# Optimization experiments

Measured on AMD Instinct MI355X. Metric: run time of the kernel, lower is better.

## Reference

```python
import jax, jax.numpy as jnp
import numpy as np

N = 4096        # nodes (cells)
E = 131072      # edges (avg degree 32)
IN = 3000       # input features (genes)
HID = 128       # hidden dim per head
H = 4           # attention heads
LAT = 16        # latent dim
NEG_SLOPE = 0.2 # PyG GATConv leaky_relu slope


def _gat_sparse(x, src, dst, W, a_src, a_dst, b, concat):
    """PyG GATConv on an edge list (src -> dst, softmax grouped by dst)."""
    n = x.shape[0]
    h_, c = a_src.shape
    h = (x @ W).reshape(n, h_, c)                      # [N,H,C]
    e_src = (h * a_src[None]).sum(-1)                  # [N,H]
    e_dst = (h * a_dst[None]).sum(-1)                  # [N,H]
    e = jax.nn.leaky_relu(e_src[src] + e_dst[dst], NEG_SLOPE)  # [E,H]
    m = jax.ops.segment_max(e, dst, num_segments=n)
    ex = jnp.exp(e - m[dst])
    denom = jax.ops.segment_sum(ex, dst, num_segments=n)
    alpha = ex / (denom[dst] + 1e-16)                  # PyG softmax eps
    out = jax.ops.segment_sum(alpha[:, :, None] * h[src], dst, num_segments=n)
    out = out.reshape(n, h_ * c) if concat else out.mean(1)
    return out + b


def _gat_dense(x, W, a_src, a_dst, b, concat):
    """GATConv over the complete graph (the SVD low-rank reconstruction is
    generically fully dense, so to_sparse() keeps all N^2 entries; with
    used_edge_weight=False only the structure matters)."""
    n = x.shape[0]
    h_, c = a_src.shape
    h = (x @ W).reshape(n, h_, c)
    e_src = (h * a_src[None]).sum(-1)                  # [N,H]
    e_dst = (h * a_dst[None]).sum(-1)                  # [N,H]
    # scores[i (target), j (source), head]
    scores = jax.nn.leaky_relu(e_dst[:, None, :] + e_src[None, :, :], NEG_SLOPE)
    alpha = jax.nn.softmax(scores, axis=1)             # softmax over sources
    out = jnp.einsum('ijh,jhc->ihc', alpha, h)
    out = out.reshape(n, h_ * c) if concat else out.mean(1)
    return out + b


def setup_inputs() -> dict:
    key = jax.random.key(0)
    ks = jax.random.split(key, 16)
    s = 0.05
    x = jax.random.normal(ks[0], (N, IN), jnp.float32)
    src = jax.random.randint(ks[1], (E,), 0, N, jnp.int32)
    off = jax.random.randint(ks[2], (E,), 1, N, jnp.int32)
    dst = (src + off) % N                              # no self loops (PyG re-adds them)
    edge_index = jnp.stack([src, dst], axis=0)
    edge_attr = jax.random.uniform(ks[3], (E,), jnp.float32)
    D1 = H * HID
    return {
        'x': x, 'edge_index': edge_index, 'edge_attr': edge_attr,
        'W1': jax.random.normal(ks[4], (IN, D1), jnp.float32) * s,
        'a1_src': jax.random.normal(ks[5], (H, HID), jnp.float32) * s,
        'a1_dst': jax.random.normal(ks[6], (H, HID), jnp.float32) * s,
        'b1': jnp.zeros((D1,), jnp.float32),
        'Wm': jax.random.normal(ks[7], (D1, H * LAT), jnp.float32) * s,
        'am_src': jax.random.normal(ks[8], (H, LAT), jnp.float32) * s,
        'am_dst': jax.random.normal(ks[9], (H, LAT), jnp.float32) * s,
        'bm': jnp.zeros((LAT,), jnp.float32),
        'Ws': jax.random.normal(ks[10], (D1, H * LAT), jnp.float32) * s,
        'as_src': jax.random.normal(ks[11], (H, LAT), jnp.float32) * s,
        'as_dst': jax.random.normal(ks[12], (H, LAT), jnp.float32) * s,
        'bs': jnp.zeros((LAT,), jnp.float32),
    }


def reference(x, edge_index, edge_attr, W1, a1_src, a1_dst, b1,
              Wm, am_src, am_dst, bm, Ws, as_src, as_dst, bs):
    loops = jnp.arange(N, dtype=edge_index.dtype)
    src = jnp.concatenate([edge_index[0], loops])      # GATConv add_self_loops=True
    dst = jnp.concatenate([edge_index[1], loops])
    # branch 1: original sparse graph
    x1 = _gat_sparse(x, src, dst, W1, a1_src, a1_dst, b1, True)
    z_mean1 = _gat_sparse(x1, src, dst, Wm, am_src, am_dst, bm, False)
    z_log_std1 = _gat_sparse(x1, src, dst, Ws, as_src, as_dst, bs, False)
    # branch 2: SVD low-rank reconstructed adjacency => complete graph
    x2 = _gat_dense(x, W1, a1_src, a1_dst, b1, True)
    z_mean2 = _gat_dense(x2, Wm, am_src, am_dst, bm, False)
    z_log_std2 = _gat_dense(x2, Ws, as_src, as_dst, bs, False)
    return (z_mean1, z_log_std1, z_mean2, z_log_std2)
```

## Files before the change

kernel.cpp:

```cpp
#include <hip/hip_runtime.h>

typedef unsigned short u16;
typedef unsigned long long u64;
typedef __attribute__((ext_vector_type(8))) short short8;
typedef __attribute__((ext_vector_type(4))) float f32x4;

#define NN   4096
#define EE   131072
#define ETOT (EE + NN)
#define HH   4
#define IND  3000
#define KP   3008
#define D1   512
#define C1   128
#define C2   16

__device__ __forceinline__ float b2f(u16 u){
  union { unsigned int i; float f; } v; v.i = ((unsigned int)u) << 16; return v.f;
}
__device__ __forceinline__ u16 f2b(float f){
  unsigned int x = __float_as_uint(f);
  unsigned int r = (x + 0x7fffu + ((x >> 16) & 1u)) >> 16;
  return (u16)r;
}
__device__ __forceinline__ float lrelu(float x){ return x > 0.f ? x : 0.2f * x; }

__device__ __forceinline__ void glds16(const void* g, void* l){
  __builtin_amdgcn_global_load_lds(
      (const __attribute__((address_space(1))) unsigned int*)g,
      (__attribute__((address_space(3))) unsigned int*)l, 16, 0, 0);
}

__global__ void zero_out_kernel(float* p, int n){
  int i = blockIdx.x * blockDim.x + threadIdx.x;
  if (i < n) p[i] = 0.f;
}

__global__ __launch_bounds__(256) void cvtXW_kernel(const float* __restrict__ X,
    const float* __restrict__ W, u16* __restrict__ Xhi, u16* __restrict__ Xlo,
    u16* __restrict__ Whi, u16* __restrict__ Wlo){
  __shared__ float T[64][65];
  int b = blockIdx.x;
  if (b < 6016){
    int id = b * 256 + threadIdx.x;
    int m = id / 376, ch = id - m * 376;
    int k = ch * 8;
    float v[8];
    if (k + 8 <= IND){
      float4 a = *(const float4*)(X + (size_t)m * IND + k);
      float4 bb = *(const float4*)(X + (size_t)m * IND + k + 4);
      v[0]=a.x; v[1]=a.y; v[2]=a.z; v[3]=a.w; v[4]=bb.x; v[5]=bb.y; v[6]=bb.z; v[7]=bb.w;
    } else {
      #pragma unroll
      for (int j = 0; j < 8; ++j){ int kk = k + j; v[j] = (kk < IND) ? X[(size_t)m*IND + kk] : 0.f; }
    }
    u16 h8[8], l8[8];
    #pragma unroll
    for (int j = 0; j < 8; ++j){ h8[j] = f2b(v[j]); l8[j] = f2b(v[j] - b2f(h8[j])); }
    *(uint4*)(Xhi + (size_t)m * KP + k) = *(uint4*)h8;
    *(uint4*)(Xlo + (size_t)m * KP + k) = *(uint4*)l8;
  } else {
    int wb = b - 6016;
    int kb = wb % 47, nb = wb / 47;
    int k0 = kb * 64, n0 = nb * 64;
    int t = threadIdx.x;
    #pragma unroll
    for (int rr = 0; rr < 4; ++rr){
      int kl = (t >> 4) + rr * 16;
      int nn = (t & 15) * 4;
      int k = k0 + kl;
      float4 v = make_float4(0.f, 0.f, 0.f, 0.f);
      if (k < IND) v = *(const float4*)(W + (size_t)k * D1 + n0 + nn);
      T[kl][nn] = v.x; T[kl][nn+1] = v.y; T[kl][nn+2] = v.z; T[kl][nn+3] = v.w;
    }
    __syncthreads();
    int nloc = t >> 2, kseg = (t & 3) * 16;
    int n = n0 + nloc;
    #pragma unroll
    for (int c2 = 0; c2 < 2; ++c2){
      int kloc = kseg + c2 * 8;
      u16 h8[8], l8[8];
      #pragma unroll
      for (int j = 0; j < 8; ++j){
        float f = T[kloc + j][nloc];
        h8[j] = f2b(f); l8[j] = f2b(f - b2f(h8[j]));
      }
      *(uint4*)(Whi + (size_t)n * KP + k0 + kloc) = *(uint4*)h8;
      *(uint4*)(Wlo + (size_t)n * KP + k0 + kloc) = *(uint4*)l8;
    }
  }
}

__global__ __launch_bounds__(256) void cvtW2_kernel(const float* __restrict__ WM,
    const float* __restrict__ WS, u16* __restrict__ Wh, u16* __restrict__ Wl){
  __shared__ float T[64][65];
  int half = blockIdx.y;
  int k0 = blockIdx.x * 64;
  const float* W = half ? WS : WM;
  int t = threadIdx.x;
  #pragma unroll
  for (int p = 0; p < 4; ++p){
    int r = p * 16 + (t >> 4), c4 = (t & 15) * 4;
    float4 v = *(const float4*)(W + (size_t)(k0 + r) * 64 + c4);
    T[r][c4] = v.x; T[r][c4+1] = v.y; T[r][c4+2] = v.z; T[r][c4+3] = v.w;
  }
  __syncthreads();
  #pragma unroll
  for (int p = 0; p < 4; ++p){
    int n = p * 16 + (t >> 4), k4 = (t & 15) * 4;
    u16 h4[4], l4[4];
    #pragma unroll
    for (int j = 0; j < 4; ++j){
      float f = T[k4 + j][n];
      h4[j] = f2b(f); l4[j] = f2b(f - b2f(h4[j]));
    }
    size_t o = (size_t)(half * 64 + n) * 512 + k0 + k4;
    *(ushort4*)(Wh + o) = *(ushort4*)h4;
    *(ushort4*)(Wl + o) = *(ushort4*)l4;
  }
}

__global__ __launch_bounds__(512) void gemm_mfma(const u16* __restrict__ Xhi,
    const u16* __restrict__ Xlo, const u16* __restrict__ Whi, const u16* __restrict__ Wlo,
    float* __restrict__ Hh){
  __shared__ u16 sbuf[2][4][4096];
  int t = threadIdx.x, lane = t & 63;
  int wv = __builtin_amdgcn_readfirstlane(t >> 6);
  int ksw = wv >> 2;
  int wr = (wv >> 1) & 1, wc = wv & 1;
  int bm = blockIdx.x * 64, bn = blockIdx.y * 64;
  f32x4 acc[2][2] = {};
  int srow = t >> 3;
  int sc = (t & 7) ^ (srow & 7);
  const char* gAh = (const char*)(Xhi + (size_t)(bm + srow) * KP) + sc * 16;
  const char* gAl = (const char*)(Xlo + (size_t)(bm + srow) * KP) + sc * 16;
  const char* gBh = (const char*)(Whi + (size_t)(bn + srow) * KP) + sc * 16;
  const char* gBl = (const char*)(Wlo + (size_t)(bn + srow) * KP) + sc * 16;
  int r16 = lane & 15, kq = lane >> 4;
  int cc = ksw * 4 + kq;
  int aoff[2], boff[2];
  #pragma unroll
  for (int m = 0; m < 2; ++m){
    int arow = wr * 32 + m * 16 + r16;
    aoff[m] = arow * 128 + ((cc ^ (arow & 7)) * 16);
  }
  #pragma unroll
  for (int n = 0; n < 2; ++n){
    int brow = wc * 32 + n * 16 + r16;
    boff[n] = brow * 128 + ((cc ^ (brow & 7)) * 16);
  }

  #define STAGE(step, b) do { int ko = (step) * 128;            \
      glds16(gAh + ko, (char*)sbuf[b][0] + t * 16);             \
      glds16(gAl + ko, (char*)sbuf[b][1] + t * 16);             \
      glds16(gBh + ko, (char*)sbuf[b][2] + t * 16);             \
      glds16(gBl + ko, (char*)sbuf[b][3] + t * 16);             \
    } while (0)
  #define BARRIER()  asm volatile("s_barrier" ::: "memory")
  #define WAIT_V4()  asm volatile("s_waitcnt vmcnt(4)" ::: "memory")
  #define WAIT_V0()  asm volatile("s_waitcnt vmcnt(0)" ::: "memory")

  STAGE(0, 0);
  STAGE(1, 1);
  WAIT_V4();
  BARRIER();
  for (int i = 0; i < 47; ++i){
    int cur = i & 1;
    const char* pAh = (const char*)sbuf[cur][0];
    const char* pAl = (const char*)sbuf[cur][1];
    const char* pBh = (const char*)sbuf[cur][2];
    const char* pBl = (const char*)sbuf[cur][3];
    short8 ah[2], al[2], bh[2], bl[2];
    #pragma unroll
    for (int m = 0; m < 2; ++m){
      ah[m] = *(const short8*)(pAh + aoff[m]);
      al[m] = *(const short8*)(pAl + aoff[m]);
    }
    #pragma unroll
    for (int n = 0; n < 2; ++n){
      bh[n] = *(const short8*)(pBh + boff[n]);
      bl[n] = *(const short8*)(pBl + boff[n]);
    }
    #pragma unroll
    for (int m = 0; m < 2; ++m)
      #pragma unroll
      for (int n = 0; n < 2; ++n){
        acc[m][n] = __builtin_amdgcn_mfma_f32_16x16x32_bf16(ah[m], bh[n], acc[m][n], 0, 0, 0);
        acc[m][n] = __builtin_amdgcn_mfma_f32_16x16x32_bf16(ah[m], bl[n], acc[m][n], 0, 0, 0);
        acc[m][n] = __builtin_amdgcn_mfma_f32_16x16x32_bf16(al[m], bh[n], acc[m][n], 0, 0, 0);
      }
    BARRIER();
    if (i + 2 < 47){
      STAGE(i + 2, cur);
      WAIT_V4();
    } else {
      WAIT_V0();
    }
    BARRIER();
  }
  #undef STAGE
  #undef BARRIER
  #undef WAIT_V4
  #undef WAIT_V0
  float* red = (float*)sbuf;
  int pp = wr * 2 + wc;
  if (ksw){
    #pragma unroll
    for (int m = 0; m < 2; ++m)
      #pragma unroll
      for (int n = 0; n < 2; ++n)
        #pragma unroll
        for (int r = 0; r < 4; ++r)
          red[((((m*2+n)*4 + r) << 8) + (pp << 6)) + lane] = acc[m][n][r];
  }
  __syncthreads();
  if (!ksw){
    #pragma unroll
    for (int m = 0; m < 2; ++m)
      #pragma unroll
      for (int n = 0; n < 2; ++n){
        #pragma unroll
        for (int r = 0; r < 4; ++r)
          acc[m][n][r] += red[((((m*2+n)*4 + r) << 8) + (pp << 6)) + lane];
        int row = bm + wr * 32 + m * 16 + kq * 4;
        int col = bn + wc * 32 + n * 16 + r16;
        float* o = Hh + (size_t)row * D1 + col;
        #pragma unroll
        for (int r = 0; r < 4; ++r) o[(size_t)r * D1] = acc[m][n][r];
      }
  }
}

__global__ __launch_bounds__(256) void gemm_h_split(const float* __restrict__ X,
    const float* __restrict__ Wc, float* __restrict__ Hh){
  __shared__ u16 Ahs[64][40], Als[64][40], Bhs[64][40], Bls[64][40];
  int t = threadIdx.x, lane = t & 63, wave = t >> 6;
  int wr = wave >> 1, wcc = wave & 1;
  int bm = blockIdx.x * 64, bn = blockIdx.y * 64;
  f32x4 acc[2][2] = {};
  int arow = t >> 2, akc = (t & 3) << 3;
  int brow = t >> 3, bnc = (t & 7) << 3;
  for (int k0 = 0; k0 < IND; k0 += 32){
    float va[8];
    size_t abase = (size_t)(bm + arow) * IND + k0 + akc;
    if (k0 + akc + 8 <= IND){
      float4 r0 = *(const float4*)(X + abase);
      float4 r1 = *(const float4*)(X + abase + 4);
      va[0]=r0.x; va[1]=r0.y; va[2]=r0.z; va[3]=r0.w;
      va[4]=r1.x; va[5]=r1.y; va[6]=r1.z; va[7]=r1.w;
    } else {
      #pragma unroll
      for (int j = 0; j < 8; ++j){
        int k = k0 + akc + j;
        va[j] = (k < IND) ? X[abase + j] : 0.f;
      }
    }
    #pragma unroll
    for (int j = 0; j < 8; ++j){
      u16 hb = f2b(va[j]);
      Ahs[arow][akc + j] = hb;
      Als[arow][akc + j] = f2b(va[j] - b2f(hb));
    }
    {
      int gk = k0 + brow;
      float vb[8];
      if (gk < IND){
        const float* wp = Wc + (size_t)gk * D1 + bn + bnc;
        float4 r0 = *(const float4*)wp;
        float4 r1 = *(const float4*)(wp + 4);
        vb[0]=r0.x; vb[1]=r0.y; vb[2]=r0.z; vb[3]=r0.w;
        vb[4]=r1.x; vb[5]=r1.y; vb[6]=r1.z; vb[7]=r1.w;
      } else {
        #pragma unroll
        for (int j = 0; j < 8; ++j) vb[j] = 0.f;
      }
      #pragma unroll
      for (int j = 0; j < 8; ++j){
        u16 hb = f2b(vb[j]);
        Bhs[bnc + j][brow] = hb;
        Bls[bnc + j][brow] = f2b(vb[j] - b2f(hb));
      }
    }
    __syncthreads();
    int r16 = lane & 15, kq = (lane >> 4) << 3;
    short8 a0h = *(const short8*)&Ahs[wr*32      + r16][kq];
    short8 a1h = *(const short8*)&Ahs[wr*32 + 16 + r16][kq];
    short8 a0l = *(const short8*)&Als[wr*32      + r16][kq];
    short8 a1l = *(const short8*)&Als[wr*32 + 16 + r16][kq];
    short8 b0h = *(const short8*)&Bhs[wcc*32      + r16][kq];
    short8 b1h = *(const short8*)&Bhs[wcc*32 + 16 + r16][kq];
    short8 b0l = *(const short8*)&Bls[wcc*32      + r16][kq];
    short8 b1l = *(const short8*)&Bls[wcc*32 + 16 + r16][kq];
    acc[0][0] = __builtin_amdgcn_mfma_f32_16x16x32_bf16(a0h, b0h, acc[0][0], 0, 0, 0);
    acc[0][1] = __builtin_amdgcn_mfma_f32_16x16x32_bf16(a0h, b1h, acc[0][1], 0, 0, 0);
    acc[1][0] = __builtin_amdgcn_mfma_f32_16x16x32_bf16(a1h, b0h, acc[1][0], 0, 0, 0);
    acc[1][1] = __builtin_amdgcn_mfma_f32_16x16x32_bf16(a1h, b1h, acc[1][1], 0, 0, 0);
    acc[0][0] = __builtin_amdgcn_mfma_f32_16x16x32_bf16(a0h, b0l, acc[0][0], 0, 0, 0);
    acc[0][1] = __builtin_amdgcn_mfma_f32_16x16x32_bf16(a0h, b1l, acc[0][1], 0, 0, 0);
    acc[1][0] = __builtin_amdgcn_mfma_f32_16x16x32_bf16(a1h, b0l, acc[1][0], 0, 0, 0);
    acc[1][1] = __builtin_amdgcn_mfma_f32_16x16x32_bf16(a1h, b1l, acc[1][1], 0, 0, 0);
    acc[0][0] = __builtin_amdgcn_mfma_f32_16x16x32_bf16(a0l, b0h, acc[0][0], 0, 0, 0);
    acc[0][1] = __builtin_amdgcn_mfma_f32_16x16x32_bf16(a0l, b1h, acc[0][1], 0, 0, 0);
    acc[1][0] = __builtin_amdgcn_mfma_f32_16x16x32_bf16(a1l, b0h, acc[1][0], 0, 0, 0);
    acc[1][1] = __builtin_amdgcn_mfma_f32_16x16x32_bf16(a1l, b1h, acc[1][1], 0, 0, 0);
    __syncthreads();
  }
  int cr = (lane >> 4) << 2, cc = lane & 15;
  for (int i = 0; i < 2; ++i) for (int j = 0; j < 2; ++j){
    int row = bm + wr*32 + i*16 + cr;
    int col = bn + wcc*32 + j*16 + cc;
    float* o = Hh + (size_t)row * D1 + col;
    for (int r = 0; r < 4; ++r) o[(size_t)r * D1] = acc[i][j][r];
  }
}

__global__ __launch_bounds__(256) void cvt_h16(const float* __restrict__ h,
    u16* __restrict__ h16){
  size_t i = ((size_t)blockIdx.x * 256 + threadIdx.x) * 8;
  float4 va = *(const float4*)(h + i);
  float4 vb = *(const float4*)(h + i + 4);
  u16 q[8] = { f2b(va.x), f2b(va.y), f2b(va.z), f2b(va.w),
               f2b(vb.x), f2b(vb.y), f2b(vb.z), f2b(vb.w) };
  *(uint4*)(h16 + i) = *(uint4*)q;
}

__global__ __launch_bounds__(256) void evec128(const float* __restrict__ hsrc,
    const float* __restrict__ as_, const float* __restrict__ ad_,
    float* __restrict__ es, float* __restrict__ ed){
  int idx = blockIdx.x * 256 + threadIdx.x;
  if (idx >= NN * HH) return;
  int h = idx & 3;
  const float4* hp = (const float4*)(hsrc + (size_t)idx * C1);
  const float4* ap = (const float4*)(as_ + h * C1);
  const float4* dp = (const float4*)(ad_ + h * C1);
  float s1 = 0.f, s2 = 0.f;
  #pragma unroll
  for (int c = 0; c < 32; ++c){
    float4 v = hp[c], a = ap[c], d = dp[c];
    s1 += v.x*a.x + v.y*a.y + v.z*a.z + v.w*a.w;
    s2 += v.x*d.x + v.y*d.y + v.z*d.z + v.w*d.w;
  }
  es[idx] = s1; ed[idx] = s2;
}

__global__ void zero_kernel(int* p, int n){
  int i = blockIdx.x * blockDim.x + threadIdx.x;
  if (i < n) p[i] = 0;
}
__global__ void hist_kernel(const int* __restrict__ dstA, int* __restrict__ deg){
  int e = blockIdx.x * blockDim.x + threadIdx.x;
  if (e < ETOT){
    int d = (e < EE) ? dstA[e] : (e - EE);
    atomicAdd(&deg[d & (NN-1)], 1);
  }
}
__global__ __launch_bounds__(1024) void scan_kernel(const int* __restrict__ deg,
    int* __restrict__ off, int* __restrict__ cur){
// ... 334 lines not shown
  float rD1 = 0.f, rD2 = 0.f;
  if (c == 0){
    size_t colD = (size_t)(sel * HH + h) * Cp + C;
    rD1 = a.T1[colD * L + pos];
    rD2 = a.T2[colD * L + pos];
  }
  size_t hb = (size_t)h * (NN + 1) + ch * CHUNK + g * KPER;
  #pragma unroll
  for (int j = 0; j < KPER; ++j){
    int kk = g * KPER + j;
    float v = hs[(size_t)PM[kk] * CW + h * C + c];
    P1[(hb + j) * Cp + c] = r1;
    P2[(hb + j) * Cp + c] = r2;
    r1 = fmaf(E1[kk], v, r1);
    r2 = fmaf(E2[kk], v, r2);
    if (c == 0){
      P1[(hb + j) * Cp + C] = rD1;
      P2[(hb + j) * Cp + C] = rD2;
      rD1 += E1[kk]; rD2 += E2[kk];
    }
  }
}

template<int C, bool MEAN>
__device__ __forceinline__ void dense_body(const float* __restrict__ P1,
    const float* __restrict__ P2, const float* __restrict__ usort,
    const float* __restrict__ ed, const float* __restrict__ bias,
    float* __restrict__ outF, u16* __restrict__ outH, u16* __restrict__ outL, int i){
  constexpr int Cp = C + 1;
  constexpr int NC = HH * C;
  int t = threadIdx.x;
  __shared__ float Ed[HH], E2d[HH], Den[HH];
  __shared__ int   Kh[HH];
  __shared__ float vals[NC > 256 ? 1 : NC];
  if (t < HH){
    float d = ed[i*HH + t];
    float target = -d;
    const float* us = usort + t * NN;
    int lo = 0, hi = NN;
    while (lo < hi){ int mid = (lo + hi) >> 1; if (us[mid] < target) lo = mid + 1; else hi = mid; }
    Kh[t] = lo;
    float e1 = __expf(d), e2 = __expf(0.2f * d);
    Ed[t] = e1; E2d[t] = e2;
    size_t base = (size_t)t * (NN + 1);
    float p1N = P1[(base + NN) * Cp + C];
    float p1k = P1[(base + lo) * Cp + C];
    float p2k = P2[(base + lo) * Cp + C];
    Den[t] = e1 * (p1N - p1k) + e2 * p2k;
  }
  __syncthreads();
  if (!MEAN){
    for (int ch = t; ch < NC; ch += 256){
      int h = ch / C, c = ch % C;
      size_t base = (size_t)h * (NN + 1);
      float p1N = P1[(base + NN)    * Cp + c];
      float p1k = P1[(base + Kh[h]) * Cp + c];
      float p2k = P2[(base + Kh[h]) * Cp + c];
      float num = Ed[h] * (p1N - p1k) + E2d[h] * p2k;
      float val = num / Den[h] + bias[ch];
      u16 hb = f2b(val);
      outH[(size_t)i * NC + ch] = hb;
      outL[(size_t)i * NC + ch] = f2b(val - b2f(hb));
    }
  } else {
    if (t < NC){
      int h = t / C, c = t % C;
      size_t base = (size_t)h * (NN + 1);
      float p1N = P1[(base + NN)    * Cp + c];
      float p1k = P1[(base + Kh[h]) * Cp + c];
      float p2k = P2[(base + Kh[h]) * Cp + c];
      vals[t] = (Ed[h] * (p1N - p1k) + E2d[h] * p2k) / Den[h];
    }
    __syncthreads();
    if (t < C){
      float z = (vals[t] + vals[C + t] + vals[2*C + t] + vals[3*C + t]) * 0.25f + bias[t];
      outF[(size_t)i * C + t] = z;
    }
  }
}

__global__ __launch_bounds__(256) void dense_out1(const float* __restrict__ P1,
    const float* __restrict__ P2, const float* __restrict__ usort,
    const float* __restrict__ ed, const float* __restrict__ bias,
    u16* __restrict__ outH, u16* __restrict__ outL){
  dense_body<C1, false>(P1, P2, usort, ed, bias, nullptr, outH, outL, blockIdx.x);
}

struct Dn2 { const float* P1[2]; const float* P2[2]; const float* us[2];
             const float* ed[2]; const float* bias[2]; float* out[2]; };
__global__ __launch_bounds__(256) void dense_out2(Dn2 a){
  int s = blockIdx.y;
  dense_body<C2, true>(a.P1[s], a.P2[s], a.us[s], a.ed[s], a.bias[s], a.out[s],
                       nullptr, nullptr, blockIdx.x);
}

extern "C" void kernel_launch(void* const* d_in, const int* in_sizes, int n_in,
                              void* d_out, int out_size, void* d_ws, size_t ws_size,
                              hipStream_t stream){
  const float* X   = (const float*)d_in[0];
  const int*   EI  = (const int*)d_in[1];
  const float* W1  = (const float*)d_in[3];
  const float* A1S = (const float*)d_in[4];
  const float* A1D = (const float*)d_in[5];
  const float* B1  = (const float*)d_in[6];
  const float* WM  = (const float*)d_in[7];
  const float* AMS = (const float*)d_in[8];
  const float* AMD = (const float*)d_in[9];
  const float* BM  = (const float*)d_in[10];
  const float* WS  = (const float*)d_in[11];
  const float* ASS = (const float*)d_in[12];
  const float* ASD = (const float*)d_in[13];
  const float* BS  = (const float*)d_in[14];
  float* OUT = (float*)d_out;
  (void)in_sizes; (void)n_in;

  if (ws_size < (size_t)56 * 1024 * 1024){
    zero_out_kernel<<<dim3((out_size + 255)/256), 256, 0, stream>>>(OUT, out_size);
    return;
  }
  bool fast = (ws_size >= (size_t)68 * 1024 * 1024);

  const size_t MB = 1024 * 1024;
  char* w = (char*)d_ws;
  size_t o = 0;
  auto alloc = [&](size_t bytes) -> void* {
    void* p = w + o;
    o += (bytes + 255) & ~(size_t)255;
    return p;
  };
  int*   deg  = (int*)  alloc(NN * 4);
  int*   coff = (int*)  alloc((NN + 1) * 4);
  int*   cur  = (int*)  alloc(NN * 4);
  int*   sidx = (int*)  alloc((size_t)ETOT * 4);
  float* e1s  = (float*)alloc(NN * HH * 4);
  float* e1d  = (float*)alloc(NN * HH * 4);
  float* us1  = (float*)alloc(HH * NN * 4);
  int*   pm1  = (int*)  alloc(HH * NN * 4);
  float* em1s = (float*)alloc(NN * HH * 4);
  float* em1d = (float*)alloc(NN * HH * 4);
  float* es1s = (float*)alloc(NN * HH * 4);
  float* es1d = (float*)alloc(NN * HH * 4);
  float* em2s = (float*)alloc(NN * HH * 4);
  float* em2d = (float*)alloc(NN * HH * 4);
  float* es2s = (float*)alloc(NN * HH * 4);
  float* es2d = (float*)alloc(NN * HH * 4);
  float* us2m = (float*)alloc(HH * NN * 4);
  int*   pm2m = (int*)  alloc(HH * NN * 4);
  float* us2s = (float*)alloc(HH * NN * 4);
  int*   pm2s = (int*)  alloc(HH * NN * 4);
  u16*   Wh2  = (u16*)  alloc(128 * 512 * 2);
  u16*   Wl2  = (u16*)  alloc(128 * 512 * 2);
  float* h    = (float*)alloc((size_t)NN * D1 * 4);
  char*  BIG  = w + o;
  size_t szX = (size_t)NN * KP * 2, szW = (size_t)D1 * KP * 2;
  u16* Xhi = (u16*)BIG;
  u16* Xlo = (u16*)(BIG + szX);
  u16* Whi = (u16*)(BIG + 2*szX);
  u16* Wlo = (u16*)(BIG + 2*szX + szW);
  u16*   x1h = (u16*)  (BIG + 0*MB);
  u16*   x1l = (u16*)  (BIG + 4*MB);
  u16*   x2h = (u16*)  (BIG + 8*MB);
  u16*   x2l = (u16*)  (BIG + 12*MB);
  float* T1a = (float*)(BIG + 16*MB);
  float* T2a = (float*)(BIG + 17*MB);
  u16*   h16 = (u16*)  (BIG + 24*MB);
  float* P1a = (float*)(BIG + 28*MB);
  float* P2a = (float*)(BIG + 37*MB);
  float* hm1  = (float*)(BIG + 16*MB);
  float* hs1  = (float*)(BIG + 17*MB);
  float* hm2  = (float*)(BIG + 18*MB);
  float* hs2  = (float*)(BIG + 19*MB);
  float* P1m  = (float*)(BIG + 20*MB);
  float* P2m  = (float*)(BIG + 21*MB + 512*1024);
  float* P1s  = (float*)(BIG + 23*MB);
  float* P2s  = (float*)(BIG + 24*MB + 512*1024);
  float* T1b  = (float*)(BIG + 26*MB);
  float* T2b  = (float*)(BIG + 26*MB + 512*1024);

  const int* srcA = EI;
  const int* dstA = EI + EE;

  cvtW2_kernel<<<dim3(8, 2), 256, 0, stream>>>(WM, WS, Wh2, Wl2);
  if (fast){
    cvtXW_kernel<<<dim3(6016 + 47*8), 256, 0, stream>>>(X, W1, Xhi, Xlo, Whi, Wlo);
    gemm_mfma<<<dim3(NN/64, D1/64), 512, 0, stream>>>(Xhi, Xlo, Whi, Wlo, h);
  } else {
    gemm_h_split<<<dim3(NN/64, D1/64), 256, 0, stream>>>(X, W1, h);
  }
  cvt_h16<<<dim3(1024), 256, 0, stream>>>(h, h16);
  evec128<<<dim3(NN*HH/256), 256, 0, stream>>>(h, A1S, A1D, e1s, e1d);
  zero_kernel<<<dim3(16), 256, 0, stream>>>(deg, NN);
  hist_kernel<<<dim3((ETOT + 255)/256), 256, 0, stream>>>(dstA, deg);
  scan_kernel<<<dim3(1), 1024, 0, stream>>>(deg, coff, cur);
  scatter_kernel<<<dim3((ETOT + 255)/256), 256, 0, stream>>>(srcA, dstA, cur, sidx);
  sparse1<<<dim3(NN), 256, 0, stream>>>(h16, e1s, e1d, coff, sidx, B1, x1h, x1l);
  {
    RkA ra; ra.in[0] = e1s; ra.in[1] = e1s; ra.us[0] = us1; ra.us[1] = us1;
    ra.pm[0] = pm1; ra.pm[1] = pm1;
    rank_kernel<<<dim3(64, 4), 1024, 0, stream>>>(ra);
    PfxN pa;
    pa.hsrc[0] = h;  pa.hsrc[1] = h;
    pa.pm[0] = pm1;  pa.pm[1] = pm1;
    pa.us[0] = us1;  pa.us[1] = us1;
    pa.T1 = T1a; pa.T2 = T2a;
    pa.P1[0] = P1a; pa.P1[1] = P1a;
    pa.P2[0] = P2a; pa.P2[1] = P2a;
    pfx_tot<C1, D1, 4, 16, 64><<<dim3(HH*64, 1), 512, 0, stream>>>(pa);
    pfx_scan<C1><<<dim3(HH*(C1+1), 1), 64, 0, stream>>>(pa, 256);
    pfx_emit<C1, D1, 4, 16, 64><<<dim3(HH*64, 1), 512, 0, stream>>>(pa);
    dense_out1<<<dim3(NN), 256, 0, stream>>>(P1a, P2a, us1, e1d, B1, x2h, x2l);
  }
  {
    GsA ga;
    ga.x1h = x1h; ga.x1l = x1l; ga.x2h = x2h; ga.x2l = x2l;
    ga.Wh = Wh2; ga.Wl = Wl2;
    ga.hm1 = hm1; ga.hs1 = hs1; ga.hm2 = hm2; ga.hs2 = hs2;
    ga.AMS = AMS; ga.AMD = AMD; ga.ASS = ASS; ga.ASD = ASD;
    ga.em1s = em1s; ga.em1d = em1d; ga.es1s = es1s; ga.es1d = es1d;
    ga.em2s = em2s; ga.em2d = em2d; ga.es2s = es2s; ga.es2d = es2d;
    gemm_small_fused<<<dim3(NN/32, 2), 256, 0, stream>>>(ga);
  }
  {
    Sp2 sp;
    sp.h[0] = hm1; sp.h[1] = hs1; sp.es[0] = em1s; sp.es[1] = es1s;
    sp.ed[0] = em1d; sp.ed[1] = es1d; sp.bias[0] = BM; sp.bias[1] = BS;
    sp.out[0] = OUT; sp.out[1] = OUT + (size_t)NN*C2;
    sparse2<<<dim3(NN, 2), 64, 0, stream>>>(sp, coff, sidx);
  }
  {
    RkA ra; ra.in[0] = em2s; ra.in[1] = es2s; ra.us[0] = us2m; ra.us[1] = us2s;
    ra.pm[0] = pm2m; ra.pm[1] = pm2s;
    rank_kernel<<<dim3(64, 8), 1024, 0, stream>>>(ra);
    PfxN pa;
    pa.hsrc[0] = hm2; pa.hsrc[1] = hs2;
    pa.pm[0] = pm2m;  pa.pm[1] = pm2s;
    pa.us[0] = us2m;  pa.us[1] = us2s;
    pa.T1 = T1b; pa.T2 = T2b;
    pa.P1[0] = P1m; pa.P1[1] = P1s;
    pa.P2[0] = P2m; pa.P2[1] = P2s;
    pfx_tot<C2, 64, 32, 8, 16><<<dim3(HH*16, 2), 512, 0, stream>>>(pa);
    pfx_scan<C2><<<dim3(HH*(C2+1), 2), 64, 0, stream>>>(pa, 512);
    pfx_emit<C2, 64, 32, 8, 16><<<dim3(HH*16, 2), 512, 0, stream>>>(pa);
    Dn2 dn;
    dn.P1[0] = P1m; dn.P1[1] = P1s; dn.P2[0] = P2m; dn.P2[1] = P2s;
    dn.us[0] = us2m; dn.us[1] = us2s; dn.ed[0] = em2d; dn.ed[1] = es2d;
    dn.bias[0] = BM; dn.bias[1] = BS;
    dn.out[0] = OUT + (size_t)2*NN*C2; dn.out[1] = OUT + (size_t)3*NN*C2;
    dense_out2<<<dim3(NN, 2), 256, 0, stream>>>(dn);
  }
}
```

Measured before the change: 353.3 us.

## Fuse fp32 X bf16 hi/lo split into MFMA GEMM load path

Removes the separate pass that converted the 4096x3000 fp32 input into padded bf16 hi and lo copies. The GEMM now streams fp32 X tiles straight into LDS and splits them into hi/lo bf16 in registers before the MFMAs, so the intermediate arrays are never written or re-read. Only W1 is still pre-split, by a smaller kernel. In exchange, A-tile LDS traffic doubles and each iteration does extra bit-manipulation. The hi part is now truncated rather than round-to-nearest, and the K tail reads past the row end, relying on zero-padded W to cancel those values.

```diff
diff --git a/kernel.cpp b/kernel.cpp
--- a/kernel.cpp
+++ b/kernel.cpp
@@ -36,58 +36,36 @@
   if (i < n) p[i] = 0.f;
 }
 
-__global__ __launch_bounds__(256) void cvtXW_kernel(const float* __restrict__ X,
-    const float* __restrict__ W, u16* __restrict__ Xhi, u16* __restrict__ Xlo,
+__global__ __launch_bounds__(256) void cvtW1_kernel(const float* __restrict__ W,
     u16* __restrict__ Whi, u16* __restrict__ Wlo){
   __shared__ float T[64][65];
-  int b = blockIdx.x;
-  if (b < 6016){
-    int id = b * 256 + threadIdx.x;
-    int m = id / 376, ch = id - m * 376;
-    int k = ch * 8;
-    float v[8];
-    if (k + 8 <= IND){
-      float4 a = *(const float4*)(X + (size_t)m * IND + k);
-      float4 bb = *(const float4*)(X + (size_t)m * IND + k + 4);
-      v[0]=a.x; v[1]=a.y; v[2]=a.z; v[3]=a.w; v[4]=bb.x; v[5]=bb.y; v[6]=bb.z; v[7]=bb.w;
-    } else {
-      #pragma unroll
-      for (int j = 0; j < 8; ++j){ int kk = k + j; v[j] = (kk < IND) ? X[(size_t)m*IND + kk] : 0.f; }
-    }
+  int wb = blockIdx.x;
+  int kb = wb % 47, nb = wb / 47;
+  int k0 = kb * 64, n0 = nb * 64;
+  int t = threadIdx.x;
+  #pragma unroll
+  for (int rr = 0; rr < 4; ++rr){
+    int kl = (t >> 4) + rr * 16;
+    int nn = (t & 15) * 4;
+    int k = k0 + kl;
+    float4 v = make_float4(0.f, 0.f, 0.f, 0.f);
+    if (k < IND) v = *(const float4*)(W + (size_t)k * D1 + n0 + nn);
+    T[kl][nn] = v.x; T[kl][nn+1] = v.y; T[kl][nn+2] = v.z; T[kl][nn+3] = v.w;
+  }
+  __syncthreads();
+  int nloc = t >> 2, kseg = (t & 3) * 16;
+  int n = n0 + nloc;
+  #pragma unroll
+  for (int c2 = 0; c2 < 2; ++c2){
+    int kloc = kseg + c2 * 8;
     u16 h8[8], l8[8];
     #pragma unroll
-    for (int j = 0; j < 8; ++j){ h8[j] = f2b(v[j]); l8[j] = f2b(v[j] - b2f(h8[j])); }
-    *(uint4*)(Xhi + (size_t)m * KP + k) = *(uint4*)h8;
-    *(uint4*)(Xlo + (size_t)m * KP + k) = *(uint4*)l8;
-  } else {
-    int wb = b - 6016;
-    int kb = wb % 47, nb = wb / 47;
-    int k0 = kb * 64, n0 = nb * 64;
-    int t = threadIdx.x;
-    #pragma unroll
-    for (int rr = 0; rr < 4; ++rr){
-      int kl = (t >> 4) + rr * 16;
-      int nn = (t & 15) * 4;
-      int k = k0 + kl;
-      float4 v = make_float4(0.f, 0.f, 0.f, 0.f);
-      if (k < IND) v = *(const float4*)(W + (size_t)k * D1 + n0 + nn);
-      T[kl][nn] = v.x; T[kl][nn+1] = v.y; T[kl][nn+2] = v.z; T[kl][nn+3] = v.w;
-    }
-    __syncthreads();
-    int nloc = t >> 2, kseg = (t & 3) * 16;
-    int n = n0 + nloc;
-    #pragma unroll
-    for (int c2 = 0; c2 < 2; ++c2){
-      int kloc = kseg + c2 * 8;
-      u16 h8[8], l8[8];
-      #pragma unroll
-      for (int j = 0; j < 8; ++j){
-        float f = T[kloc + j][nloc];
-        h8[j] = f2b(f); l8[j] = f2b(f - b2f(h8[j]));
-      }
-      *(uint4*)(Whi + (size_t)n * KP + k0 + kloc) = *(uint4*)h8;
-      *(uint4*)(Wlo + (size_t)n * KP + k0 + kloc) = *(uint4*)l8;
-    }
+    for (int j = 0; j < 8; ++j){
+      float f = T[kloc + j][nloc];
+      h8[j] = f2b(f); l8[j] = f2b(f - b2f(h8[j]));
+    }
+    *(uint4*)(Whi + (size_t)n * KP + k0 + kloc) = *(uint4*)h8;
+    *(uint4*)(Wlo + (size_t)n * KP + k0 + kloc) = *(uint4*)l8;
   }
 }
 
@@ -120,29 +98,34 @@
   }
 }
 
-__global__ __launch_bounds__(512) void gemm_mfma(const u16* __restrict__ Xhi,
-    const u16* __restrict__ Xlo, const u16* __restrict__ Whi, const u16* __restrict__ Wlo,
+__global__ __launch_bounds__(512) void gemm_mfma(const float* __restrict__ Xf,
+    const u16* __restrict__ Whi, const u16* __restrict__ Wlo,
     float* __restrict__ Hh){
-  __shared__ u16 sbuf[2][4][4096];
+  __shared__ char smem[2][32768];
   int t = threadIdx.x, lane = t & 63;
   int wv = __builtin_amdgcn_readfirstlane(t >> 6);
   int ksw = wv >> 2;
   int wr = (wv >> 1) & 1, wc = wv & 1;
   int bm = blockIdx.x * 64, bn = blockIdx.y * 64;
   f32x4 acc[2][2] = {};
-  int srow = t >> 3;
-  int sc = (t & 7) ^ (srow & 7);
-  const char* gAh = (const char*)(Xhi + (size_t)(bm + srow) * KP) + sc * 16;
-  const char* gAl = (const char*)(Xlo + (size_t)(bm + srow) * KP) + sc * 16;
-  const char* gBh = (const char*)(Whi + (size_t)(bn + srow) * KP) + sc * 16;
-  const char* gBl = (const char*)(Wlo + (size_t)(bn + srow) * KP) + sc * 16;
+  int ar0 = t >> 4,        ac0 = (t & 15) ^ (ar0 & 15);
+  int ar1 = 32 + (t >> 4), ac1 = (t & 15) ^ (ar1 & 15);
+  const char* gA0 = (const char*)(Xf + (size_t)(bm + ar0) * IND) + ac0 * 16;
+  const char* gA1 = (const char*)(Xf + (size_t)(bm + ar1) * IND) + ac1 * 16;
+  const char* gAmax = (const char*)Xf + (size_t)NN * IND * 4 - 16;
+  int bsr = t >> 3;
+  int bsc = (t & 7) ^ (bsr & 7);
+  const char* gBh = (const char*)(Whi + (size_t)(bn + bsr) * KP) + bsc * 16;
+  const char* gBl = (const char*)(Wlo + (size_t)(bn + bsr) * KP) + bsc * 16;
   int r16 = lane & 15, kq = lane >> 4;
   int cc = ksw * 4 + kq;
-  int aoff[2], boff[2];
+  int aoff0[2], aoff1[2], boff[2];
   #pragma unroll
   for (int m = 0; m < 2; ++m){
     int arow = wr * 32 + m * 16 + r16;
-    aoff[m] = arow * 128 + ((cc ^ (arow & 7)) * 16);
+    int c0 = cc * 2, c1 = cc * 2 + 1;
+    aoff0[m] = arow * 256 + ((c0 ^ (arow & 15)) * 16);
+    aoff1[m] = arow * 256 + ((c1 ^ (arow & 15)) * 16);
   }
   #pragma unroll
   for (int n = 0; n < 2; ++n){
@@ -150,11 +133,13 @@
     boff[n] = brow * 128 + ((cc ^ (brow & 7)) * 16);
   }
 
-  #define STAGE(step, b) do { int ko = (step) * 128;            \
-      glds16(gAh + ko, (char*)sbuf[b][0] + t * 16);             \
-      glds16(gAl + ko, (char*)sbuf[b][1] + t * 16);             \
-      glds16(gBh + ko, (char*)sbuf[b][2] + t * 16);             \
-      glds16(gBl + ko, (char*)sbuf[b][3] + t * 16);             \
+  #define STAGE(step, b) do {                                           \
+      const char* pa0 = gA0 + (step) * 256; if (pa0 > gAmax) pa0 = gAmax; \
+      const char* pa1 = gA1 + (step) * 256; if (pa1 > gAmax) pa1 = gAmax; \
+      glds16(pa0, smem[b] + t * 16);                                    \
+      glds16(pa1, smem[b] + (t + 512) * 16);                            \
+      glds16(gBh + (step) * 128, smem[b] + 16384 + t * 16);             \
+      glds16(gBl + (step) * 128, smem[b] + 24576 + t * 16);             \
     } while (0)
   #define BARRIER()  asm volatile("s_barrier" ::: "memory")
   #define WAIT_V4()  asm volatile("s_waitcnt vmcnt(4)" ::: "memory")
@@ -166,15 +151,28 @@
   BARRIER();
   for (int i = 0; i < 47; ++i){
     int cur = i & 1;
-    const char* pAh = (const char*)sbuf[cur][0];
-    const char* pAl = (const char*)sbuf[cur][1];
-    const char* pBh = (const char*)sbuf[cur][2];
-    const char* pBl = (const char*)sbuf[cur][3];
+    const char* pA  = smem[cur];
+    const char* pBh = smem[cur] + 16384;
+    const char* pBl = smem[cur] + 24576;
     short8 ah[2], al[2], bh[2], bl[2];
     #pragma unroll
     for (int m = 0; m < 2; ++m){
-      ah[m] = *(const short8*)(pAh + aoff[m]);
-      al[m] = *(const short8*)(pAl + aoff[m]);
+      float4 fa = *(const float4*)(pA + aoff0[m]);
+      float4 fb = *(const float4*)(pA + aoff1[m]);
+      float f[8] = { fa.x, fa.y, fa.z, fa.w, fb.x, fb.y, fb.z, fb.w };
+      unsigned hw[4], lw[4];
+      #pragma unroll
+      for (int p = 0; p < 4; ++p){
+        unsigned u0 = __float_as_uint(f[2*p]);
+        unsigned u1 = __float_as_uint(f[2*p+1]);
+        unsigned m0 = u0 & 0xffff0000u, m1 = u1 & 0xffff0000u;
+        hw[p] = (m0 >> 16) | m1;
+        float l0 = f[2*p]   - __uint_as_float(m0);
+        float l1 = f[2*p+1] - __uint_as_float(m1);
+        lw[p] = (__float_as_uint(l0) >> 16) | (__float_as_uint(l1) & 0xffff0000u);
+      }
+      ah[m] = *(short8*)hw;
+      al[m] = *(short8*)lw;
     }
     #pragma unroll
     for (int n = 0; n < 2; ++n){
@@ -202,7 +200,7 @@
   #undef BARRIER
   #undef WAIT_V4
   #undef WAIT_V0
-  float* red = (float*)sbuf;
+  float* red = (float*)smem;
   int pp = wr * 2 + wc;
   if (ksw){
     #pragma unroll
@@ -843,11 +841,8 @@
   u16*   Wl2  = (u16*)  alloc(128 * 512 * 2);
   float* h    = (float*)alloc((size_t)NN * D1 * 4);
   char*  BIG  = w + o;
-  size_t szX = (size_t)NN * KP * 2, szW = (size_t)D1 * KP * 2;
-  u16* Xhi = (u16*)BIG;
-  u16* Xlo = (u16*)(BIG + szX);
-  u16* Whi = (u16*)(BIG + 2*szX);
-  u16* Wlo = (u16*)(BIG + 2*szX + szW);
+  u16* Whi = (u16*)BIG;
+  u16* Wlo = (u16*)(BIG + 4*MB);
   u16*   x1h = (u16*)  (BIG + 0*MB);
   u16*   x1l = (u16*)  (BIG + 4*MB);
   u16*   x2h = (u16*)  (BIG + 8*MB);
@@ -873,8 +868,8 @@
 
   cvtW2_kernel<<<dim3(8, 2), 256, 0, stream>>>(WM, WS, Wh2, Wl2);
   if (fast){
-    cvtXW_kernel<<<dim3(6016 + 47*8), 256, 0, stream>>>(X, W1, Xhi, Xlo, Whi, Wlo);
-    gemm_mfma<<<dim3(NN/64, D1/64), 512, 0, stream>>>(Xhi, Xlo, Whi, Wlo, h);
+    cvtW1_kernel<<<dim3(47*8), 256, 0, stream>>>(W1, Whi, Wlo);
+    gemm_mfma<<<dim3(NN/64, D1/64), 512, 0, stream>>>(X, Whi, Wlo, h);
   } else {
     gemm_h_split<<<dim3(NN/64, D1/64), 256, 0, stream>>>(X, W1, h);
   }
```

Measured after the change: 354.7 us. Within noise of the previous version (+0.4%).

## Fuse X fp32-to-bf16 hi/lo split into GEMM A-tile staging

Applied to the files above, without the earlier changes.

Removes the separate pass that converted the 4096x3000 fp32 input into padded bf16 hi/lo copies. The GEMM now loads fp32 X rows into registers one step ahead, splits them into hi/lo bf16 in-kernel with perm ops, and writes them to LDS. W is still staged into LDS asynchronously. This saves a large write-then-reread of converted X. In exchange, each column block repeats the conversion, and the A path loses its async LDS loads. The K tail is handled by clamping the pointer, which reads neighbouring data that is cancelled by zero-padded W; completion of the B loads now relies on compiler-inserted waits.

```diff
diff --git a/kernel.cpp b/kernel.cpp
--- a/kernel.cpp
+++ b/kernel.cpp
@@ -36,58 +36,36 @@
   if (i < n) p[i] = 0.f;
 }
 
-__global__ __launch_bounds__(256) void cvtXW_kernel(const float* __restrict__ X,
-    const float* __restrict__ W, u16* __restrict__ Xhi, u16* __restrict__ Xlo,
+__global__ __launch_bounds__(256) void cvtW1_kernel(const float* __restrict__ W,
     u16* __restrict__ Whi, u16* __restrict__ Wlo){
   __shared__ float T[64][65];
-  int b = blockIdx.x;
-  if (b < 6016){
-    int id = b * 256 + threadIdx.x;
-    int m = id / 376, ch = id - m * 376;
-    int k = ch * 8;
-    float v[8];
-    if (k + 8 <= IND){
-      float4 a = *(const float4*)(X + (size_t)m * IND + k);
-      float4 bb = *(const float4*)(X + (size_t)m * IND + k + 4);
-      v[0]=a.x; v[1]=a.y; v[2]=a.z; v[3]=a.w; v[4]=bb.x; v[5]=bb.y; v[6]=bb.z; v[7]=bb.w;
-    } else {
-      #pragma unroll
-      for (int j = 0; j < 8; ++j){ int kk = k + j; v[j] = (kk < IND) ? X[(size_t)m*IND + kk] : 0.f; }
-    }
+  int wb = blockIdx.x;
+  int kb = wb % 47, nb = wb / 47;
+  int k0 = kb * 64, n0 = nb * 64;
+  int t = threadIdx.x;
+  #pragma unroll
+  for (int rr = 0; rr < 4; ++rr){
+    int kl = (t >> 4) + rr * 16;
+    int nn = (t & 15) * 4;
+    int k = k0 + kl;
+    float4 v = make_float4(0.f, 0.f, 0.f, 0.f);
+    if (k < IND) v = *(const float4*)(W + (size_t)k * D1 + n0 + nn);
+    T[kl][nn] = v.x; T[kl][nn+1] = v.y; T[kl][nn+2] = v.z; T[kl][nn+3] = v.w;
+  }
+  __syncthreads();
+  int nloc = t >> 2, kseg = (t & 3) * 16;
+  int n = n0 + nloc;
+  #pragma unroll
+  for (int c2 = 0; c2 < 2; ++c2){
+    int kloc = kseg + c2 * 8;
     u16 h8[8], l8[8];
     #pragma unroll
-    for (int j = 0; j < 8; ++j){ h8[j] = f2b(v[j]); l8[j] = f2b(v[j] - b2f(h8[j])); }
-    *(uint4*)(Xhi + (size_t)m * KP + k) = *(uint4*)h8;
-    *(uint4*)(Xlo + (size_t)m * KP + k) = *(uint4*)l8;
-  } else {
-    int wb = b - 6016;
-    int kb = wb % 47, nb = wb / 47;
-    int k0 = kb * 64, n0 = nb * 64;
-    int t = threadIdx.x;
-    #pragma unroll
-    for (int rr = 0; rr < 4; ++rr){
-      int kl = (t >> 4) + rr * 16;
-      int nn = (t & 15) * 4;
-      int k = k0 + kl;
-      float4 v = make_float4(0.f, 0.f, 0.f, 0.f);
-      if (k < IND) v = *(const float4*)(W + (size_t)k * D1 + n0 + nn);
-      T[kl][nn] = v.x; T[kl][nn+1] = v.y; T[kl][nn+2] = v.z; T[kl][nn+3] = v.w;
-    }
-    __syncthreads();
-    int nloc = t >> 2, kseg = (t & 3) * 16;
-    int n = n0 + nloc;
-    #pragma unroll
-    for (int c2 = 0; c2 < 2; ++c2){
-      int kloc = kseg + c2 * 8;
-      u16 h8[8], l8[8];
-      #pragma unroll
-      for (int j = 0; j < 8; ++j){
-        float f = T[kloc + j][nloc];
-        h8[j] = f2b(f); l8[j] = f2b(f - b2f(h8[j]));
-      }
-      *(uint4*)(Whi + (size_t)n * KP + k0 + kloc) = *(uint4*)h8;
-      *(uint4*)(Wlo + (size_t)n * KP + k0 + kloc) = *(uint4*)l8;
-    }
+    for (int j = 0; j < 8; ++j){
+      float f = T[kloc + j][nloc];
+      h8[j] = f2b(f); l8[j] = f2b(f - b2f(h8[j]));
+    }
+    *(uint4*)(Whi + (size_t)n * KP + k0 + kloc) = *(uint4*)h8;
+    *(uint4*)(Wlo + (size_t)n * KP + k0 + kloc) = *(uint4*)l8;
   }
 }
 
@@ -120,8 +98,8 @@
   }
 }
 
-__global__ __launch_bounds__(512) void gemm_mfma(const u16* __restrict__ Xhi,
-    const u16* __restrict__ Xlo, const u16* __restrict__ Whi, const u16* __restrict__ Wlo,
+__global__ __launch_bounds__(512) void gemm_mfma(const float* __restrict__ Xf,
+    const u16* __restrict__ Whi, const u16* __restrict__ Wlo,
     float* __restrict__ Hh){
   __shared__ u16 sbuf[2][4][4096];
   int t = threadIdx.x, lane = t & 63;
@@ -132,8 +110,8 @@
   f32x4 acc[2][2] = {};
   int srow = t >> 3;
   int sc = (t & 7) ^ (srow & 7);
-  const char* gAh = (const char*)(Xhi + (size_t)(bm + srow) * KP) + sc * 16;
-  const char* gAl = (const char*)(Xlo + (size_t)(bm + srow) * KP) + sc * 16;
+  const char* gA  = (const char*)(Xf + (size_t)(bm + srow) * IND) + sc * 32;
+  const char* gAend = (const char*)Xf + (size_t)NN * IND * 4 - 16;
   const char* gBh = (const char*)(Whi + (size_t)(bn + srow) * KP) + sc * 16;
   const char* gBl = (const char*)(Wlo + (size_t)(bn + srow) * KP) + sc * 16;
   int r16 = lane & 15, kq = lane >> 4;
@@ -150,19 +128,46 @@
     boff[n] = brow * 128 + ((cc ^ (brow & 7)) * 16);
   }
 
-  #define STAGE(step, b) do { int ko = (step) * 128;            \
-      glds16(gAh + ko, (char*)sbuf[b][0] + t * 16);             \
-      glds16(gAl + ko, (char*)sbuf[b][1] + t * 16);             \
-      glds16(gBh + ko, (char*)sbuf[b][2] + t * 16);             \
-      glds16(gBl + ko, (char*)sbuf[b][3] + t * 16);             \
+  float4 ra0, ra1;
+  #define LOADA(step) do {                                      \
+      const char* p0 = gA + (step) * 256;                       \
+      const char* p1 = p0 + 16;                                 \
+      if (p0 > gAend) p0 = gAend;                               \
+      if (p1 > gAend) p1 = gAend;                               \
+      ra0 = *(const float4*)p0;                                 \
+      ra1 = *(const float4*)p1;                                 \
+    } while (0)
+  #define WRITEA(b) do {                                        \
+      float ff[8] = { ra0.x, ra0.y, ra0.z, ra0.w,               \
+                      ra1.x, ra1.y, ra1.z, ra1.w };             \
+      unsigned hw[4], lw[4];                                    \
+      _Pragma("unroll")                                         \
+      for (int p = 0; p < 4; ++p){                              \
+        unsigned u0 = __float_as_uint(ff[2*p]);                 \
+        unsigned u1 = __float_as_uint(ff[2*p+1]);               \
+        hw[p] = __builtin_amdgcn_perm(u1, u0, 0x07060302u);     \
+        float l0 = ff[2*p]   - __uint_as_float(u0 & 0xffff0000u); \
+        float l1 = ff[2*p+1] - __uint_as_float(u1 & 0xffff0000u); \
+        lw[p] = __builtin_amdgcn_perm(__float_as_uint(l1),      \
+                                      __float_as_uint(l0), 0x07060302u); \
+      }                                                         \
+      *(uint4*)((char*)sbuf[b][0] + t * 16) = *(uint4*)hw;      \
+      *(uint4*)((char*)sbuf[b][1] + t * 16) = *(uint4*)lw;      \
+    } while (0)
+  #define GLDSB(step, b) do {                                   \
+      glds16(gBh + (step) * 128, (char*)sbuf[b][2] + t * 16);   \
+      glds16(gBl + (step) * 128, (char*)sbuf[b][3] + t * 16);   \
     } while (0)
   #define BARRIER()  asm volatile("s_barrier" ::: "memory")
-  #define WAIT_V4()  asm volatile("s_waitcnt vmcnt(4)" ::: "memory")
-  #define WAIT_V0()  asm volatile("s_waitcnt vmcnt(0)" ::: "memory")
-
-  STAGE(0, 0);
-  STAGE(1, 1);
-  WAIT_V4();
+
+  LOADA(0);
+  WRITEA(0);
+  LOADA(1);
+  GLDSB(0, 0);
+  GLDSB(1, 1);
+  WRITEA(1);
+  LOADA(2);
+  asm volatile("s_waitcnt vmcnt(2) lgkmcnt(0)" ::: "memory");
   BARRIER();
   for (int i = 0; i < 47; ++i){
     int cur = i & 1;
@@ -191,17 +196,19 @@
       }
     BARRIER();
     if (i + 2 < 47){
-      STAGE(i + 2, cur);
-      WAIT_V4();
+      WRITEA(cur);
+      GLDSB(i + 2, cur);
+      if (i + 3 < 47) LOADA(i + 3);
+      asm volatile("s_waitcnt lgkmcnt(0)" ::: "memory");
     } else {
-      WAIT_V0();
+      asm volatile("s_waitcnt vmcnt(0) lgkmcnt(0)" ::: "memory");
     }
     BARRIER();
   }
-  #undef STAGE
+  #undef LOADA
+  #undef WRITEA
+  #undef GLDSB
   #undef BARRIER
-  #undef WAIT_V4
-  #undef WAIT_V0
   float* red = (float*)sbuf;
   int pp = wr * 2 + wc;
   if (ksw){
@@ -843,11 +850,8 @@
   u16*   Wl2  = (u16*)  alloc(128 * 512 * 2);
   float* h    = (float*)alloc((size_t)NN * D1 * 4);
   char*  BIG  = w + o;
-  size_t szX = (size_t)NN * KP * 2, szW = (size_t)D1 * KP * 2;
-  u16* Xhi = (u16*)BIG;
-  u16* Xlo = (u16*)(BIG + szX);
-  u16* Whi = (u16*)(BIG + 2*szX);
-  u16* Wlo = (u16*)(BIG + 2*szX + szW);
+  u16* Whi = (u16*)BIG;
+  u16* Wlo = (u16*)(BIG + 4*MB);
   u16*   x1h = (u16*)  (BIG + 0*MB);
   u16*   x1l = (u16*)  (BIG + 4*MB);
   u16*   x2h = (u16*)  (BIG + 8*MB);
@@ -873,8 +877,8 @@
 
   cvtW2_kernel<<<dim3(8, 2), 256, 0, stream>>>(WM, WS, Wh2, Wl2);
   if (fast){
-    cvtXW_kernel<<<dim3(6016 + 47*8), 256, 0, stream>>>(X, W1, Xhi, Xlo, Whi, Wlo);
-    gemm_mfma<<<dim3(NN/64, D1/64), 512, 0, stream>>>(Xhi, Xlo, Whi, Wlo, h);
+    cvtW1_kernel<<<dim3(47*8), 256, 0, stream>>>(W1, Whi, Wlo);
+    gemm_mfma<<<dim3(NN/64, D1/64), 512, 0, stream>>>(X, Whi, Wlo, h);
   } else {
     gemm_h_split<<<dim3(NN/64, D1/64), 256, 0, stream>>>(X, W1, h);
   }
```

New measurement: 347.7 us. No clear change (-1.6%).
